# Kernel optimization log

Measured on AMD Instinct MI355X. Metric: run time of the kernel, lower is better.

The kernel has to match this reference:

```python
import jax, jax.numpy as jnp
import numpy as np

M_INST = 64   # num_instances (labels 1..64; 0 = background)
L_ANCH = 8    # anchors per instance
C_DIM = 256   # anchor_dim == embed dim (num_mapping_layers=0, num_heads=1)
B, H, W = 8, 64, 64


def setup_inputs() -> dict:
    key = jax.random.key(0)
    ks = jax.random.split(key, 7)
    s = 1.0 / np.sqrt(C_DIM)
    return {
        "anchors": jax.random.normal(ks[0], (M_INST, L_ANCH, C_DIM), jnp.float32),
        "features": jax.random.normal(ks[1], (B, H, W, C_DIM), jnp.float32),
        "instances_in_view": jax.random.randint(ks[2], (B, H, W), 0, M_INST + 1, jnp.int32),
        # nn.MultiheadAttention packed in-projection and out-projection params
        "in_proj_w": jax.random.normal(ks[3], (3 * C_DIM, C_DIM), jnp.float32) * s,
        "in_proj_b": jax.random.normal(ks[4], (3 * C_DIM,), jnp.float32) * s,
        "out_w": jax.random.normal(ks[5], (C_DIM, C_DIM), jnp.float32) * s,
        "out_b": jax.random.normal(ks[6], (C_DIM,), jnp.float32) * s,
    }


def reference(anchors, features, instances_in_view, in_proj_w, in_proj_b, out_w, out_b):
    # Cross-attention anchor_type, Identity maps (num_mapping_layers=0, num_heads=1).
    # Each pixel (query) attends to the L anchors of its instance; padding in the
    # original pad_sequence pipeline never affects non-pad queries, so the
    # gather/pack -> MHA -> unmap -> residual-add pipeline reduces to per-pixel math.
    C = anchors.shape[-1]
    Wq, Wk, Wv = in_proj_w[:C], in_proj_w[C:2 * C], in_proj_w[2 * C:]
    bq, bk, bv = in_proj_b[:C], in_proj_b[C:2 * C], in_proj_b[2 * C:]

    # Project keys/values once per instance: (M, L, C)
    K = jnp.einsum('mlc,dc->mld', anchors, Wk) + bk
    V = jnp.einsum('mlc,dc->mld', anchors, Wv) + bv

    Bsz, Hh, Ww, _ = features.shape
    f = features.reshape(-1, C)                       # (N, C)
    lab = instances_in_view.reshape(-1)               # (N,) labels 0..M
    idx = jnp.maximum(lab - 1, 0)                     # anchor row per pixel

    q = f @ Wq.T + bq                                 # (N, C)
    Kg = K[idx]                                       # (N, L, C) irregular gather
    Vg = V[idx]                                       # (N, L, C)

    scale = 1.0 / np.sqrt(C).astype(np.float32)
    scores = jnp.einsum('nc,nlc->nl', q, Kg) * scale  # (N, L)
    attn = jax.nn.softmax(scores, axis=-1)
    o = jnp.einsum('nl,nlc->nc', attn, Vg)            # (N, C)
    o = o @ out_w.T + out_b                           # MHA out_proj

    # background (label 0) pixels get zero anchor feature; residual add
    o = jnp.where((lab > 0)[:, None], o, jnp.zeros((), o.dtype))
    out = f + o
    return out.reshape(Bsz, Hh, Ww, C)
```

## Files before the change

kernel.cpp:

```cpp
#include <hip/hip_runtime.h>
#include <stdint.h>

#define C_DIM   256
#define L_ANCH  8
#define M_INST  64
#define NPIX    32768
#define LDSTR   264
#define WSTR    40
#define TSTR    80

typedef __attribute__((ext_vector_type(8))) short  short8;
typedef __attribute__((ext_vector_type(4))) float  float4v;

__device__ __forceinline__ float bf2f(unsigned short b) {
    union { unsigned u; float f; } x; x.u = ((unsigned)b) << 16; return x.f;
}
__device__ __forceinline__ unsigned short f2bf(float f) {
    union { unsigned u; float f; } x; x.f = f;
    unsigned u = x.u;
    return (unsigned short)((u + 0x7FFFu + ((u >> 16) & 1u)) >> 16);
}
__device__ __forceinline__ ushort4 f4bf(float4 f) {
    ushort4 v; v.x = f2bf(f.x); v.y = f2bf(f.y); v.z = f2bf(f.z); v.w = f2bf(f.w);
    return v;
}

__global__ __launch_bounds__(256) void prep1_kernel(
    const float* __restrict__ anchors, const float* __restrict__ in_proj_w,
    const float* __restrict__ in_proj_b, const float* __restrict__ out_w,
    unsigned short* __restrict__ Kb, unsigned short* __restrict__ Vb,
    unsigned short* __restrict__ WqT, unsigned short* __restrict__ Owb)
{
    __shared__ unsigned short Abuf[32 * LDSTR];
    __shared__ unsigned short Wtile[4][32 * WSTR];
    __shared__ unsigned short Ttile[64 * TSTR];
    const int b = blockIdx.x, t = threadIdx.x;

    if (b >= 128) {
        const int tidx = b - 128;
        const int r0 = (tidx >> 2) * 64, c0 = (tidx & 3) * 64;
#pragma unroll
        for (int i = 0; i < 4; ++i) {
            int id = t + i * 256;
            int row = id >> 4, c4 = id & 15;
            float4 f = *(const float4*)&in_proj_w[(size_t)(r0 + row) * C_DIM + c0 + c4 * 4];
            Ttile[(c4 * 4 + 0) * TSTR + row] = f2bf(f.x);
            Ttile[(c4 * 4 + 1) * TSTR + row] = f2bf(f.y);
            Ttile[(c4 * 4 + 2) * TSTR + row] = f2bf(f.z);
            Ttile[(c4 * 4 + 3) * TSTR + row] = f2bf(f.w);
        }
        __syncthreads();
#pragma unroll
        for (int i = 0; i < 2; ++i) {
            int id = t + i * 256;
            int cc = id >> 3, ch = id & 7;
            *(short8*)&WqT[(size_t)(c0 + cc) * C_DIM + r0 + ch * 8] =
                *(const short8*)&Ttile[cc * TSTR + ch * 8];
        }
        return;
    }

    if (b >= 64) {
        const int id = (b - 64) * 256 + t;
        float4 f = *((const float4*)out_w + id);
        *((ushort4*)Owb + id) = f4bf(f);
        return;
    }

    const int mat = b >> 5, tile = (b >> 1) & 15, half = b & 1;
    const int m0 = tile * 32;
#pragma unroll
    for (int i = 0; i < 8; ++i) {
        int id = t + i * 256;
        int row = id >> 6, c4 = id & 63;
        float4 f = *((const float4*)(anchors + (size_t)(m0 + row) * C_DIM) + c4);
        *(ushort4*)&Abuf[row * LDSTR + c4 * 4] = f4bf(f);
    }
    __syncthreads();

    const int wave = t >> 6, lane = t & 63, r16 = lane & 15, quad = lane >> 4;
    const int colbase = half * 128 + wave * 32;
    const int wbase = C_DIM + mat * C_DIM + colbase;
    unsigned short* Wl = &Wtile[wave][0];

    float4v acc[2][2];
#pragma unroll
    for (int mt = 0; mt < 2; ++mt)
#pragma unroll
        for (int nt = 0; nt < 2; ++nt)
#pragma unroll
            for (int r = 0; r < 4; ++r) acc[mt][nt][r] = 0.f;

    for (int ks = 0; ks < 8; ++ks) {
        const int rr = lane >> 3, cc = lane & 7;
#pragma unroll
        for (int i = 0; i < 4; ++i) {
            int row = rr + i * 8;
            float4 f = *((const float4*)(in_proj_w + (size_t)(wbase + row) * C_DIM + ks * 32) + cc);
            *(ushort4*)&Wl[row * WSTR + cc * 4] = f4bf(f);
        }
        const int c0 = ks * 32 + quad * 8;
        short8 afr[2], bfr[2];
#pragma unroll
        for (int mt = 0; mt < 2; ++mt)
            afr[mt] = *(const short8*)&Abuf[(mt * 16 + r16) * LDSTR + c0];
#pragma unroll
        for (int nt = 0; nt < 2; ++nt)
            bfr[nt] = *(const short8*)&Wl[(nt * 16 + r16) * WSTR + quad * 8];
#pragma unroll
        for (int mt = 0; mt < 2; ++mt)
#pragma unroll
            for (int nt = 0; nt < 2; ++nt)
                acc[mt][nt] = __builtin_amdgcn_mfma_f32_16x16x32_bf16(
                    afr[mt], bfr[nt], acc[mt][nt], 0, 0, 0);
    }

    unsigned short* dst = mat ? Vb : Kb;
#pragma unroll
    for (int nt = 0; nt < 2; ++nt) {
        const int col = colbase + nt * 16 + r16;
        const float bias = in_proj_b[C_DIM + mat * C_DIM + col];
#pragma unroll
        for (int mt = 0; mt < 2; ++mt)
#pragma unroll
            for (int r = 0; r < 4; ++r) {
                int row = m0 + mt * 16 + quad * 4 + r;
                dst[(size_t)row * C_DIM + col] = f2bf(acc[mt][nt][r] + bias);
            }
    }
}

__global__ __launch_bounds__(256) void prep2_kernel(
    const unsigned short* __restrict__ Kb, const unsigned short* __restrict__ Vb,
    const unsigned short* __restrict__ WqT, const unsigned short* __restrict__ Owb,
    const float* __restrict__ in_proj_b,
    unsigned short* __restrict__ G, unsigned short* __restrict__ U,
    float* __restrict__ g0)
{
    __shared__ unsigned short Abuf[32 * LDSTR];
    const int b = blockIdx.x, t = threadIdx.x;
    const int isG = (b < 32) ? 1 : 0;
    const int tile = (b >> 1) & 15, half = b & 1;
    const int m0 = tile * 32;
    const unsigned short* src = isG ? Kb : Vb;
    const unsigned short* W   = isG ? WqT : Owb;
    unsigned short* dst       = isG ? G : U;

#pragma unroll
    for (int i = 0; i < 4; ++i) {
        int id = t + i * 256;
        int row = id >> 5, c8 = id & 31;
        *(short8*)&Abuf[row * LDSTR + c8 * 8] =
            *(const short8*)&src[(size_t)(m0 + row) * C_DIM + c8 * 8];
    }
    __syncthreads();

    const int wave = t >> 6, lane = t & 63, r16 = lane & 15, quad = lane >> 4;

    if (isG && half == 0) {
        const int grow = t >> 3, gs = t & 7;
        float gp = 0.f;
#pragma unroll
        for (int c = 0; c < 32; ++c)
            gp += bf2f(Abuf[grow * LDSTR + gs * 32 + c]) * in_proj_b[gs * 32 + c];
        gp += __shfl_down(gp, 1);
        gp += __shfl_down(gp, 2);
        gp += __shfl_down(gp, 4);
        if (gs == 0) g0[m0 + grow] = gp;
    }

    const int colbase = half * 128 + wave * 32;

    float4v acc[2][2];
#pragma unroll
    for (int mt = 0; mt < 2; ++mt)
#pragma unroll
        for (int nt = 0; nt < 2; ++nt)
#pragma unroll
            for (int r = 0; r < 4; ++r) acc[mt][nt][r] = 0.f;

    for (int ks = 0; ks < 8; ++ks) {
        const int c0 = ks * 32 + quad * 8;
        short8 afr[2], bfr[2];
#pragma unroll
        for (int mt = 0; mt < 2; ++mt)
            afr[mt] = *(const short8*)&Abuf[(mt * 16 + r16) * LDSTR + c0];
#pragma unroll
        for (int nt = 0; nt < 2; ++nt)
            bfr[nt] = *(const short8*)&W[(size_t)(colbase + nt * 16 + r16) * C_DIM + c0];
#pragma unroll
        for (int mt = 0; mt < 2; ++mt)
#pragma unroll
            for (int nt = 0; nt < 2; ++nt)
                acc[mt][nt] = __builtin_amdgcn_mfma_f32_16x16x32_bf16(
                    afr[mt], bfr[nt], acc[mt][nt], 0, 0, 0);
    }

#pragma unroll
    for (int nt = 0; nt < 2; ++nt) {
        const int col = colbase + nt * 16 + r16;
#pragma unroll
        for (int mt = 0; mt < 2; ++mt)
#pragma unroll
            for (int r = 0; r < 4; ++r) {
                int row = m0 + mt * 16 + quad * 4 + r;
                dst[(size_t)row * C_DIM + col] = f2bf(acc[mt][nt][r]);
            }
    }
}

__global__ __launch_bounds__(256) void gather_kernel(
    const float* __restrict__ features, const int* __restrict__ inst,
    const float* __restrict__ out_b,
    const unsigned short* __restrict__ G, const unsigned short* __restrict__ U,
    const float* __restrict__ g0, float* __restrict__ out)
{
    const int t = threadIdx.x;
    const int p = t >> 4, s = t & 15;
    const int n = blockIdx.x * 16 + p;
    const int lab = inst[n];
    const int m = max(lab - 1, 0);
    const unsigned short* Gp = G + (size_t)m * (L_ANCH * C_DIM) + s * 16;
    const unsigned short* Up = U + (size_t)m * (L_ANCH * C_DIM) + s * 16;

    float fr[16];
    const float4* fp = (const float4*)(features + (size_t)n * C_DIM + s * 16);
#pragma unroll
    for (int i = 0; i < 4; ++i) *(float4*)&fr[i * 4] = fp[i];

    float sc[L_ANCH];
#pragma unroll
    for (int l = 0; l < L_ANCH; ++l) {
        short8 gv0 = *(const short8*)(Gp + l * C_DIM);
        short8 gv1 = *(const short8*)(Gp + l * C_DIM + 8);
        float a0 = 0.f, a1 = 0.f;
#pragma unroll
        for (int j = 0; j < 8; ++j) {
            a0 += bf2f(((const unsigned short*)&gv0)[j]) * fr[j];
            a1 += bf2f(((const unsigned short*)&gv1)[j]) * fr[8 + j];
        }
        float partial = a0 + a1;
        partial += __shfl_down(partial, 1);
        partial += __shfl_down(partial, 2);
        partial += __shfl_down(partial, 4);
        partial += __shfl_down(partial, 8);
        sc[l] = partial;
    }

    float attn[L_ANCH];
    if (s == 0) {
        const float scale = 0.0625f;
        float mx = -1e30f;
#pragma unroll
        for (int l = 0; l < L_ANCH; ++l) {
            sc[l] = (sc[l] + g0[m * L_ANCH + l]) * scale;
            mx = fmaxf(mx, sc[l]);
        }
        float sum = 0.f;
#pragma unroll
        for (int l = 0; l < L_ANCH; ++l) { attn[l] = __expf(sc[l] - mx); sum += attn[l]; }
        float inv = 1.f / sum;
#pragma unroll
        for (int l = 0; l < L_ANCH; ++l) attn[l] *= inv;
    }
    const int base_lane = (t & 63) & ~15;
    float a_bc[L_ANCH];
#pragma unroll
    for (int l = 0; l < L_ANCH; ++l) a_bc[l] = __shfl(attn[l], base_lane);

    float y[16];
#pragma unroll
    for (int c = 0; c < 16; ++c) y[c] = 0.f;
#pragma unroll
    for (int l = 0; l < L_ANCH; ++l) {
        const float av = a_bc[l];
        short8 uv0 = *(const short8*)(Up + l * C_DIM);
        short8 uv1 = *(const short8*)(Up + l * C_DIM + 8);
#pragma unroll
        for (int j = 0; j < 8; ++j) {
            y[j]     += av * bf2f(((const unsigned short*)&uv0)[j]);
            y[8 + j] += av * bf2f(((const unsigned short*)&uv1)[j]);
        }
    }

    const float fm = (lab > 0) ? 1.f : 0.f;
    float4* op = (float4*)(out + (size_t)n * C_DIM + s * 16);
    const float4* obp = (const float4*)(out_b + s * 16);
#pragma unroll
    for (int i = 0; i < 4; ++i) {
        float4 ob = obp[i];
        float4 o;
        o.x = fr[i * 4 + 0] + fm * (y[i * 4 + 0] + ob.x);
        o.y = fr[i * 4 + 1] + fm * (y[i * 4 + 1] + ob.y);
        o.z = fr[i * 4 + 2] + fm * (y[i * 4 + 2] + ob.z);
        o.w = fr[i * 4 + 3] + fm * (y[i * 4 + 3] + ob.w);
        op[i] = o;
    }
}

extern "C" void kernel_launch(void* const* d_in, const int* in_sizes, int n_in,
                              void* d_out, int out_size, void* d_ws, size_t ws_size,
                              hipStream_t stream) {
    const float* anchors   = (const float*)d_in[0];
    const float* features  = (const float*)d_in[1];
    const int*   inst      = (const int*)d_in[2];
    const float* in_proj_w = (const float*)d_in[3];
    const float* in_proj_b = (const float*)d_in[4];
    const float* out_w     = (const float*)d_in[5];
    const float* out_b     = (const float*)d_in[6];
    float* out = (float*)d_out;

    unsigned short* Kb  = (unsigned short*)d_ws;
    unsigned short* Vb  = Kb  + M_INST * L_ANCH * C_DIM;
    unsigned short* WqT = Vb  + M_INST * L_ANCH * C_DIM;
    unsigned short* Owb = WqT + C_DIM * C_DIM;
    unsigned short* G   = Owb + C_DIM * C_DIM;
    unsigned short* U   = G   + M_INST * L_ANCH * C_DIM;
    float*          g0  = (float*)(U + M_INST * L_ANCH * C_DIM);

    prep1_kernel<<<144, 256, 0, stream>>>(anchors, in_proj_w, in_proj_b, out_w,
                                          Kb, Vb, WqT, Owb);
    prep2_kernel<<<64, 256, 0, stream>>>(Kb, Vb, WqT, Owb, in_proj_b, G, U, g0);
    gather_kernel<<<NPIX / 16, 256, 0, stream>>>(features, inst, out_b, G, U, g0, out);
}
```

Before: 120.6 us.

## Interleave G/U tables, fold weight conversion into GEMM loads, simplify softmax reduction

G and U are now stored in one interleaved table with 512-wide rows, so each pixel's gather reads one contiguous region per anchor instead of two separate tables. The softmax uses xor-butterfly reductions so every lane computes the attention weights itself, which removes the broadcast shuffles. In the prep kernels the LDS staging and the standalone out_w conversion pass are dropped, and bf16 conversion now happens directly in the fp32 MFMA operand loads. The gather kernel also gets an occupancy hint, in exchange for somewhat less coalesced global loads inside the small prep GEMMs.

```diff
diff --git a/kernel.cpp b/kernel.cpp
--- a/kernel.cpp
+++ b/kernel.cpp
@@ -6,8 +6,8 @@
 #define M_INST  64
 #define NPIX    32768
 #define LDSTR   264
-#define WSTR    40
 #define TSTR    80
+#define GUSTR   512
 
 typedef __attribute__((ext_vector_type(8))) short  short8;
 typedef __attribute__((ext_vector_type(4))) float  float4v;
@@ -24,20 +24,24 @@
     ushort4 v; v.x = f2bf(f.x); v.y = f2bf(f.y); v.z = f2bf(f.z); v.w = f2bf(f.w);
     return v;
 }
+__device__ __forceinline__ short8 f8bf(float4 a, float4 b) {
+    union { short8 v; ushort4 q[2]; } u;
+    u.q[0] = f4bf(a); u.q[1] = f4bf(b);
+    return u.v;
+}
 
 __global__ __launch_bounds__(256) void prep1_kernel(
     const float* __restrict__ anchors, const float* __restrict__ in_proj_w,
-    const float* __restrict__ in_proj_b, const float* __restrict__ out_w,
+    const float* __restrict__ in_proj_b,
     unsigned short* __restrict__ Kb, unsigned short* __restrict__ Vb,
-    unsigned short* __restrict__ WqT, unsigned short* __restrict__ Owb)
+    unsigned short* __restrict__ WqT)
 {
     __shared__ unsigned short Abuf[32 * LDSTR];
-    __shared__ unsigned short Wtile[4][32 * WSTR];
     __shared__ unsigned short Ttile[64 * TSTR];
     const int b = blockIdx.x, t = threadIdx.x;
 
-    if (b >= 128) {
-        const int tidx = b - 128;
+    if (b >= 64) {
+        const int tidx = b - 64;
         const int r0 = (tidx >> 2) * 64, c0 = (tidx & 3) * 64;
 #pragma unroll
         for (int i = 0; i < 4; ++i) {
@@ -60,13 +64,6 @@
         return;
     }
 
-    if (b >= 64) {
-        const int id = (b - 64) * 256 + t;
-        float4 f = *((const float4*)out_w + id);
-        *((ushort4*)Owb + id) = f4bf(f);
-        return;
-    }
-
     const int mat = b >> 5, tile = (b >> 1) & 15, half = b & 1;
     const int m0 = tile * 32;
 #pragma unroll
@@ -81,7 +78,6 @@
     const int wave = t >> 6, lane = t & 63, r16 = lane & 15, quad = lane >> 4;
     const int colbase = half * 128 + wave * 32;
     const int wbase = C_DIM + mat * C_DIM + colbase;
-    unsigned short* Wl = &Wtile[wave][0];
 
     float4v acc[2][2];
 #pragma unroll
@@ -91,22 +87,18 @@
 #pragma unroll
             for (int r = 0; r < 4; ++r) acc[mt][nt][r] = 0.f;
 
+#pragma unroll
     for (int ks = 0; ks < 8; ++ks) {
-        const int rr = lane >> 3, cc = lane & 7;
-#pragma unroll
-        for (int i = 0; i < 4; ++i) {
-            int row = rr + i * 8;
-            float4 f = *((const float4*)(in_proj_w + (size_t)(wbase + row) * C_DIM + ks * 32) + cc);
-            *(ushort4*)&Wl[row * WSTR + cc * 4] = f4bf(f);
-        }
         const int c0 = ks * 32 + quad * 8;
         short8 afr[2], bfr[2];
 #pragma unroll
         for (int mt = 0; mt < 2; ++mt)
             afr[mt] = *(const short8*)&Abuf[(mt * 16 + r16) * LDSTR + c0];
 #pragma unroll
-        for (int nt = 0; nt < 2; ++nt)
-            bfr[nt] = *(const short8*)&Wl[(nt * 16 + r16) * WSTR + quad * 8];
+        for (int nt = 0; nt < 2; ++nt) {
+            const float* wrow = in_proj_w + (size_t)(wbase + nt * 16 + r16) * C_DIM + c0;
+            bfr[nt] = f8bf(*(const float4*)wrow, *(const float4*)(wrow + 4));
+        }
 #pragma unroll
         for (int mt = 0; mt < 2; ++mt)
 #pragma unroll
@@ -132,37 +124,31 @@
 
 __global__ __launch_bounds__(256) void prep2_kernel(
     const unsigned short* __restrict__ Kb, const unsigned short* __restrict__ Vb,
-    const unsigned short* __restrict__ WqT, const unsigned short* __restrict__ Owb,
+    const unsigned short* __restrict__ WqT, const float* __restrict__ out_w,
     const float* __restrict__ in_proj_b,
-    unsigned short* __restrict__ G, unsigned short* __restrict__ U,
-    float* __restrict__ g0)
+    unsigned short* __restrict__ GU, float* __restrict__ g0)
 {
-    __shared__ unsigned short Abuf[32 * LDSTR];
     const int b = blockIdx.x, t = threadIdx.x;
     const int isG = (b < 32) ? 1 : 0;
     const int tile = (b >> 1) & 15, half = b & 1;
     const int m0 = tile * 32;
     const unsigned short* src = isG ? Kb : Vb;
-    const unsigned short* W   = isG ? WqT : Owb;
-    unsigned short* dst       = isG ? G : U;
-
-#pragma unroll
-    for (int i = 0; i < 4; ++i) {
-        int id = t + i * 256;
-        int row = id >> 5, c8 = id & 31;
-        *(short8*)&Abuf[row * LDSTR + c8 * 8] =
-            *(const short8*)&src[(size_t)(m0 + row) * C_DIM + c8 * 8];
-    }
-    __syncthreads();
+    const int ucol = isG ? 0 : 256;
 
     const int wave = t >> 6, lane = t & 63, r16 = lane & 15, quad = lane >> 4;
 
     if (isG && half == 0) {
         const int grow = t >> 3, gs = t & 7;
+        const unsigned short* kr = Kb + (size_t)(m0 + grow) * C_DIM + gs * 32;
         float gp = 0.f;
 #pragma unroll
-        for (int c = 0; c < 32; ++c)
-            gp += bf2f(Abuf[grow * LDSTR + gs * 32 + c]) * in_proj_b[gs * 32 + c];
+        for (int c8 = 0; c8 < 4; ++c8) {
+            short8 kv = *(const short8*)(kr + c8 * 8);
+            const float* bp = in_proj_b + gs * 32 + c8 * 8;
+#pragma unroll
+            for (int j = 0; j < 8; ++j)
+                gp += bf2f((unsigned short)kv[j]) * bp[j];
+        }
         gp += __shfl_down(gp, 1);
         gp += __shfl_down(gp, 2);
         gp += __shfl_down(gp, 4);
@@ -179,15 +165,23 @@
 #pragma unroll
             for (int r = 0; r < 4; ++r) acc[mt][nt][r] = 0.f;
 
+#pragma unroll
     for (int ks = 0; ks < 8; ++ks) {
         const int c0 = ks * 32 + quad * 8;
         short8 afr[2], bfr[2];
 #pragma unroll
         for (int mt = 0; mt < 2; ++mt)
-            afr[mt] = *(const short8*)&Abuf[(mt * 16 + r16) * LDSTR + c0];
-#pragma unroll
-        for (int nt = 0; nt < 2; ++nt)
-            bfr[nt] = *(const short8*)&W[(size_t)(colbase + nt * 16 + r16) * C_DIM + c0];
+            afr[mt] = *(const short8*)&src[(size_t)(m0 + mt * 16 + r16) * C_DIM + c0];
+#pragma unroll
+        for (int nt = 0; nt < 2; ++nt) {
+            const int wr = colbase + nt * 16 + r16;
+            if (isG) {
+                bfr[nt] = *(const short8*)&WqT[(size_t)wr * C_DIM + c0];
+            } else {
+                const float* wp = out_w + (size_t)wr * C_DIM + c0;
+                bfr[nt] = f8bf(*(const float4*)wp, *(const float4*)(wp + 4));
+            }
+        }
 #pragma unroll
         for (int mt = 0; mt < 2; ++mt)
 #pragma unroll
@@ -204,24 +198,23 @@
 #pragma unroll
             for (int r = 0; r < 4; ++r) {
                 int row = m0 + mt * 16 + quad * 4 + r;
-                dst[(size_t)row * C_DIM + col] = f2bf(acc[mt][nt][r]);
+                GU[(size_t)row * GUSTR + ucol + col] = f2bf(acc[mt][nt][r]);
             }
     }
 }
 
-__global__ __launch_bounds__(256) void gather_kernel(
+__global__ __launch_bounds__(256, 4) void gather_kernel(
     const float* __restrict__ features, const int* __restrict__ inst,
     const float* __restrict__ out_b,
-    const unsigned short* __restrict__ G, const unsigned short* __restrict__ U,
-    const float* __restrict__ g0, float* __restrict__ out)
+    const unsigned short* __restrict__ GU, const float* __restrict__ g0,
+    float* __restrict__ out)
 {
     const int t = threadIdx.x;
     const int p = t >> 4, s = t & 15;
     const int n = blockIdx.x * 16 + p;
     const int lab = inst[n];
     const int m = max(lab - 1, 0);
-    const unsigned short* Gp = G + (size_t)m * (L_ANCH * C_DIM) + s * 16;
-    const unsigned short* Up = U + (size_t)m * (L_ANCH * C_DIM) + s * 16;
+    const unsigned short* GUp = GU + (size_t)m * (L_ANCH * GUSTR) + s * 16;
 
     float fr[16];
     const float4* fp = (const float4*)(features + (size_t)n * C_DIM + s * 16);
@@ -229,57 +222,54 @@
     for (int i = 0; i < 4; ++i) *(float4*)&fr[i * 4] = fp[i];
 
     float sc[L_ANCH];
+    short8 uv0[L_ANCH];
 #pragma unroll
     for (int l = 0; l < L_ANCH; ++l) {
-        short8 gv0 = *(const short8*)(Gp + l * C_DIM);
-        short8 gv1 = *(const short8*)(Gp + l * C_DIM + 8);
+        const unsigned short* rp = GUp + l * GUSTR;
+        short8 gv0 = *(const short8*)rp;
+        short8 gv1 = *(const short8*)(rp + 8);
+        uv0[l] = *(const short8*)(rp + 256);
         float a0 = 0.f, a1 = 0.f;
 #pragma unroll
         for (int j = 0; j < 8; ++j) {
-            a0 += bf2f(((const unsigned short*)&gv0)[j]) * fr[j];
-            a1 += bf2f(((const unsigned short*)&gv1)[j]) * fr[8 + j];
-        }
-        float partial = a0 + a1;
-        partial += __shfl_down(partial, 1);
-        partial += __shfl_down(partial, 2);
-        partial += __shfl_down(partial, 4);
-        partial += __shfl_down(partial, 8);
-        sc[l] = partial;
-    }
-
-    float attn[L_ANCH];
-    if (s == 0) {
-        const float scale = 0.0625f;
-        float mx = -1e30f;
-#pragma unroll
-        for (int l = 0; l < L_ANCH; ++l) {
-            sc[l] = (sc[l] + g0[m * L_ANCH + l]) * scale;
-            mx = fmaxf(mx, sc[l]);
-        }
-        float sum = 0.f;
-#pragma unroll
-        for (int l = 0; l < L_ANCH; ++l) { attn[l] = __expf(sc[l] - mx); sum += attn[l]; }
-        float inv = 1.f / sum;
-#pragma unroll
-        for (int l = 0; l < L_ANCH; ++l) attn[l] *= inv;
-    }
-    const int base_lane = (t & 63) & ~15;
-    float a_bc[L_ANCH];
-#pragma unroll
-    for (int l = 0; l < L_ANCH; ++l) a_bc[l] = __shfl(attn[l], base_lane);
+            a0 += bf2f((unsigned short)gv0[j]) * fr[j];
+            a1 += bf2f((unsigned short)gv1[j]) * fr[8 + j];
+        }
+        sc[l] = a0 + a1;
+    }
+
+    const float4 g0a = *(const float4*)&g0[m * L_ANCH];
+    const float4 g0b = *(const float4*)&g0[m * L_ANCH + 4];
+    const float gb[L_ANCH] = {g0a.x, g0a.y, g0a.z, g0a.w, g0b.x, g0b.y, g0b.z, g0b.w};
+
+    float mx = -1e30f;
+#pragma unroll
+    for (int l = 0; l < L_ANCH; ++l) {
+        float v = sc[l];
+        v += __shfl_xor(v, 1);
+        v += __shfl_xor(v, 2);
+        v += __shfl_xor(v, 4);
+        v += __shfl_xor(v, 8);
+        v = (v + gb[l]) * 0.0625f;
+        sc[l] = v;
+        mx = fmaxf(mx, v);
+    }
+    float sum = 0.f;
+#pragma unroll
+    for (int l = 0; l < L_ANCH; ++l) { sc[l] = __expf(sc[l] - mx); sum += sc[l]; }
+    const float inv = 1.f / sum;
 
     float y[16];
 #pragma unroll
     for (int c = 0; c < 16; ++c) y[c] = 0.f;
 #pragma unroll
     for (int l = 0; l < L_ANCH; ++l) {
-        const float av = a_bc[l];
-        short8 uv0 = *(const short8*)(Up + l * C_DIM);
-        short8 uv1 = *(const short8*)(Up + l * C_DIM + 8);
+        const float av = sc[l] * inv;
+        short8 u1 = *(const short8*)(GUp + l * GUSTR + 264);
 #pragma unroll
         for (int j = 0; j < 8; ++j) {
-            y[j]     += av * bf2f(((const unsigned short*)&uv0)[j]);
-            y[8 + j] += av * bf2f(((const unsigned short*)&uv1)[j]);
+            y[j]     += av * bf2f((unsigned short)uv0[l][j]);
+            y[8 + j] += av * bf2f((unsigned short)u1[j]);
         }
     }
 
@@ -313,13 +303,10 @@
     unsigned short* Kb  = (unsigned short*)d_ws;
     unsigned short* Vb  = Kb  + M_INST * L_ANCH * C_DIM;
     unsigned short* WqT = Vb  + M_INST * L_ANCH * C_DIM;
-    unsigned short* Owb = WqT + C_DIM * C_DIM;
-    unsigned short* G   = Owb + C_DIM * C_DIM;
-    unsigned short* U   = G   + M_INST * L_ANCH * C_DIM;
-    float*          g0  = (float*)(U + M_INST * L_ANCH * C_DIM);
-
-    prep1_kernel<<<144, 256, 0, stream>>>(anchors, in_proj_w, in_proj_b, out_w,
-                                          Kb, Vb, WqT, Owb);
-    prep2_kernel<<<64, 256, 0, stream>>>(Kb, Vb, WqT, Owb, in_proj_b, G, U, g0);
-    gather_kernel<<<NPIX / 16, 256, 0, stream>>>(features, inst, out_b, G, U, g0, out);
-}
+    unsigned short* GU  = WqT + C_DIM * C_DIM;
+    float*          g0  = (float*)(GU + M_INST * L_ANCH * GUSTR);
+
+    prep1_kernel<<<80, 256, 0, stream>>>(anchors, in_proj_w, in_proj_b, Kb, Vb, WqT);
+    prep2_kernel<<<64, 256, 0, stream>>>(Kb, Vb, WqT, out_w, in_proj_b, GU, g0);
+    gather_kernel<<<NPIX / 16, 256, 0, stream>>>(features, inst, out_b, GU, g0, out);
+}
```

After: 234.0 us. +94.0%, slower.
